# Kernel tuning notes

Measured on AMD Instinct MI355X. Metric: run time of the kernel, lower is better.

## Reference

```python
import jax, jax.numpy as jnp
import numpy as np

B_, L_, O_, N_, S_, U_, DEL, HID, K = 16, 128, 128, 256, 64, 32, 64, 512, 4
D_OUT = DEL + N_ * U_ + N_ * S_  # 24640


def setup_inputs() -> dict:
    key = jax.random.key(0)
    ks = jax.random.split(key, 12)
    return {
        "x": jax.random.normal(ks[0], (B_, O_ + L_, S_), jnp.float32),
        "u": jax.random.normal(ks[1], (B_, 2 * L_, U_), jnp.float32),
        "A": jax.random.normal(ks[2], (N_, 1), jnp.float32) / 20.0,
        "W0": jax.random.normal(ks[3], (HID, S_), jnp.float32) * 0.05,
        "b0": jnp.zeros((HID,), jnp.float32),
        "W1": jax.random.normal(ks[4], (N_, HID), jnp.float32) * 0.05,
        "b1": jnp.zeros((N_,), jnp.float32),
        "conv_w": jax.random.normal(ks[5], (N_ + U_, 1, K), jnp.float32) * 0.3,
        "conv_b": jnp.zeros((N_ + U_,), jnp.float32),
        "Wg": jax.random.normal(ks[6], (D_OUT, N_ + U_), jnp.float32) * 0.05,
        "bg": jnp.zeros((D_OUT,), jnp.float32),
        "Wdt": jax.random.normal(ks[7], (N_, DEL), jnp.float32) * 0.05,
        "bdt": jnp.zeros((N_,), jnp.float32),
    }


def reference(x, u, A, W0, b0, W1, b1, conv_w, conv_b, Wg, bg, Wdt, bdt):
    def proj_x(v):  # Linear -> relu -> Linear (project_x)
        return jax.nn.relu(v @ W0.T + b0) @ W1.T + b1

    u = u[:, :, :U_]
    z0 = proj_x(x[:, O_ - 1, :])                       # (B, N)

    # ---- generate_matrices ----
    x_all = proj_x(x[:, :O_ - 1, :])                   # (B, O-1, N)
    u_all = u[:, :O_ - 1, :]                           # (B, O-1, U)
    old = jax.nn.silu(jnp.concatenate([x_all, u_all], axis=2))  # (B, O-1, N+U)
    old = jnp.transpose(old, (0, 2, 1))                # (B, N+U, O-1)
    old = jax.lax.conv_general_dilated(
        old, conv_w, window_strides=(1,), padding=[(K - 1, K - 1)],
        dimension_numbers=("NCH", "OIH", "NCH"), feature_group_count=N_ + U_,
    ) + conv_b[None, :, None]
    old = old[:, :, -L_:]                              # last L timesteps
    old = jax.nn.silu(jnp.transpose(old, (0, 2, 1)))   # (B, L, N+U)
    gen = old @ Wg.T + bg                              # (B, L, delta + N*U + N*S)
    delta, Bm, Cm = jnp.split(gen, [DEL, DEL + N_ * U_], axis=-1)
    delta = jax.nn.softplus(delta @ Wdt.T + bdt)       # (B, L, N)
    Bm = Bm.reshape(B_, L_, N_, U_)
    Cm = Cm.reshape(B_, L_, N_, S_)

    # ---- discretion_matrices ----
    a = A[:, 0]
    a = -jnp.where(a > 0, a, jnp.expm1(a))             # -celu(A), alpha=1
    dA = jnp.exp(delta * a)                            # (B, L, N)
    dB = ((dA - 1.0) * (1.0 / a))[..., None] * Bm      # (B, L, N, U)

    # ---- selective_scan ----
    u0 = u[:, O_ - 1:O_ - 1 + L_, :]                   # (B, L, U)
    xt = x[:, O_:O_ + L_, :]                           # (B, L, S) targets

    def step(z, inp):
        dAi, dBi, ui, Ci, xti = inp
        z = z * dAi + jnp.einsum("bnu,bu->bn", dBi, ui)
        y = jnp.einsum("bns,bn->bs", Ci, z)
        return z, (y, jnp.mean((y - xti) ** 2))

    xs = (
        jnp.swapaxes(dA, 0, 1), jnp.swapaxes(dB, 0, 1),
        jnp.swapaxes(u0, 0, 1), jnp.swapaxes(Cm, 0, 1), jnp.swapaxes(xt, 0, 1),
    )
    _, (ys, ls) = jax.lax.scan(step, z0, xs)
    loss = jnp.sum(ls) / L_
    return loss, jax.lax.stop_gradient(ys)             # ys: (L, B, S), detached as in torch
```

## Files before the change

### kernel.cpp

```cpp
#include <hip/hip_runtime.h>
#include <math.h>

#define B_   16
#define L_   128
#define O_   128
#define N_   256
#define S_   64
#define U_   32
#define DEL_ 64
#define HID_ 512
#define CH_  288
#define M_   2048
#define KD_  288
#define CM_BASE (DEL_ + N_*U_)
#define NSLICE 32

typedef __bf16 bf16_t;
typedef bf16_t bf16x8 __attribute__((ext_vector_type(8)));
typedef float  f32x4  __attribute__((ext_vector_type(4)));

#define AS1(p) ((const __attribute__((address_space(1))) void*)(unsigned long long)(const void*)(p))
#define AS3(p) ((__attribute__((address_space(3))) void*)(unsigned int)(unsigned long long)(const void*)(p))

__device__ __forceinline__ float silu_f(float x){ return x / (1.f + expf(-x)); }
__device__ __forceinline__ float softplus_f(float x){
  return fmaxf(x, 0.f) + log1pf(expf(-fabsf(x)));
}

__device__ __forceinline__ void cvt8(const float* src, bf16_t* dst){
  float4 a = ((const float4*)src)[0];
  float4 b = ((const float4*)src)[1];
  bf16x8 o;
  o[0]=(bf16_t)a.x; o[1]=(bf16_t)a.y; o[2]=(bf16_t)a.z; o[3]=(bf16_t)a.w;
  o[4]=(bf16_t)b.x; o[5]=(bf16_t)b.y; o[6]=(bf16_t)b.z; o[7]=(bf16_t)b.w;
  *(bf16x8*)dst = o;
}

#define CVT_BLOCKS 3465
#define W0_BLOCKS  16
#define W1_BLOCKS  64
#define XB_BLOCKS  64
#define WGT_BLOCKS 72
__global__ void k_prep(const float* __restrict__ Wg, bf16_t* __restrict__ Wgbf,
                       const float* __restrict__ W0, bf16_t* __restrict__ W0bf,
                       const float* __restrict__ W1, bf16_t* __restrict__ W1bf,
                       const float* __restrict__ x,  bf16_t* __restrict__ xbf,
                       float* __restrict__ WgdT, float* __restrict__ lossa){
  if (blockIdx.x == 0 && threadIdx.x < 2) lossa[threadIdx.x] = 0.f;
  if (blockIdx.x < CVT_BLOCKS) {
    int i = blockIdx.x*256 + threadIdx.x;
    if (i >= 887040) return;
    cvt8(Wg + (size_t)i*8, Wgbf + (size_t)i*8);
  } else if (blockIdx.x < CVT_BLOCKS + W0_BLOCKS) {
    int i = (blockIdx.x - CVT_BLOCKS)*256 + threadIdx.x;
    if (i >= 4096) return;
    cvt8(W0 + (size_t)i*8, W0bf + (size_t)i*8);
  } else if (blockIdx.x < CVT_BLOCKS + W0_BLOCKS + W1_BLOCKS) {
    int i = (blockIdx.x - CVT_BLOCKS - W0_BLOCKS)*256 + threadIdx.x;
    if (i >= 16384) return;
    cvt8(W1 + (size_t)i*8, W1bf + (size_t)i*8);
  } else if (blockIdx.x < CVT_BLOCKS + W0_BLOCKS + W1_BLOCKS + XB_BLOCKS) {
    int i = (blockIdx.x - CVT_BLOCKS - W0_BLOCKS - W1_BLOCKS)*256 + threadIdx.x;
    if (i >= 16384) return;
    int m = i >> 3, c0 = (i & 7)*8;
    int b = m >> 7, t = m & 127;
    cvt8(x + (size_t)(((b<<8)+t)<<6) + c0, xbf + (size_t)m*64 + c0);
  } else {
    int i = (blockIdx.x - CVT_BLOCKS - W0_BLOCKS - W1_BLOCKS - XB_BLOCKS)*256 + threadIdx.x;
    if (i >= 18432) return;
    int d = i / KD_, k = i - d*KD_;
    WgdT[k*64 + d] = Wg[(size_t)d*KD_ + k];
  }
}

#define STAGE64K(GBASE, ROW0G, STRIDE, KK, LDSP)                                     \
  { const bf16_t* gp_ = (GBASE) + (size_t)((ROW0G) + wave*16 + lm)*(STRIDE) + (KK) + lq*8; \
    __builtin_amdgcn_global_load_lds(AS1(gp_), AS3((LDSP) + wave*512), 16, 0, 0); }

#define STAGE128(GBASE, ROW0G, STRIDE, TT, BUF)                                      \
  { _Pragma("unroll")                                                                \
    for (int kb_ = 0; kb_ < 4; kb_++) {                                              \
      const bf16_t* gp_ = (GBASE) + (size_t)((ROW0G) + wave*16 + lm)*(STRIDE)        \
                          + (TT)*128 + kb_*32 + lq*8;                                \
      __builtin_amdgcn_global_load_lds(AS1(gp_), AS3((BUF) + kb_*2048 + wave*512), 16, 0, 0);\
    } }

#define STAGE32(GBASE, ROW0G, KK, LDSP)                                              \
  { _Pragma("unroll")                                                                \
    for (int l_ = 0; l_ < 2; l_++) {                                                 \
      int g_ = wave*2 + l_;                                                          \
      const bf16_t* gp_ = (GBASE) + (size_t)((ROW0G) + g_*16 + lm)*KD_ + (KK) + lq*8;\
      __builtin_amdgcn_global_load_lds(AS1(gp_), AS3((LDSP) + g_*512), 16, 0, 0);    \
    } }

#define STAGE_FR96(GBASE, ROW0G, KK, LDSP)                                           \
  { _Pragma("unroll")                                                                \
    for (int c_ = 0; c_ < 3; c_++) {                                                 \
      _Pragma("unroll")                                                              \
      for (int q_ = 0; q_ < 2; q_++) {                                               \
        int g_ = wave*2 + q_;                                                        \
        const bf16_t* gp_ = (GBASE) + (size_t)((ROW0G) + g_*16 + lm)*KD_ + (KK) + c_*32 + lq*8;\
        __builtin_amdgcn_global_load_lds(AS1(gp_), AS3((LDSP) + c_*4096 + g_*512), 16, 0, 0);\
      } } }

__global__ __launch_bounds__(256) void k_mlp1m(
    const bf16_t* __restrict__ xbf, const bf16_t* __restrict__ W0bf,
    const float* __restrict__ b0, bf16_t* __restrict__ Hbf){
  __shared__ __align__(16) bf16_t As[2][2048];
  __shared__ __align__(16) bf16_t Bs[2][2048];
  int tid = threadIdx.x;
  int wave = tid >> 6, lane = tid & 63;
  int wm = wave & 1, wn = wave >> 1;
  int nt = blockIdx.x, mt = blockIdx.y;
  int m0 = mt*64, n0 = nt*64;
  int lm = lane & 15, lq = lane >> 4;

  f32x4 acc[2][2];
  #pragma unroll
  for (int i=0;i<2;i++)
    #pragma unroll
    for (int j=0;j<2;j++){ acc[i][j][0]=0.f;acc[i][j][1]=0.f;acc[i][j][2]=0.f;acc[i][j][3]=0.f; }

  STAGE64K(xbf,  m0, 64, 0, As[0]);
  STAGE64K(W0bf, n0, 64, 0, Bs[0]);
  __syncthreads();
  #pragma unroll
  for (int t = 0; t < 2; ++t) {
    int cur = t & 1;
    if (t < 1) {
      STAGE64K(xbf,  m0, 64, 32, As[1]);
      STAGE64K(W0bf, n0, 64, 32, Bs[1]);
    }
    bf16x8 af[2], bff[2];
    #pragma unroll
    for (int i=0;i<2;i++) af[i]  = *(const bf16x8*)&As[cur][(wm*2 + i)*512 + lane*8];
    #pragma unroll
    for (int j=0;j<2;j++) bff[j] = *(const bf16x8*)&Bs[cur][(wn*2 + j)*512 + lane*8];
    #pragma unroll
    for (int i=0;i<2;i++)
      #pragma unroll
      for (int j=0;j<2;j++)
        acc[i][j] = __builtin_amdgcn_mfma_f32_16x16x32_bf16(af[i], bff[j], acc[i][j], 0,0,0);
    __syncthreads();
  }
  #pragma unroll
  for (int i=0;i<2;i++)
    #pragma unroll
    for (int j=0;j<2;j++){
      int col = n0 + wn*32 + j*16 + lm;
      float bb = b0[col];
      #pragma unroll
      for (int r=0;r<4;r++){
        int row = m0 + wm*32 + i*16 + lq*4 + r;
        Hbf[(size_t)row*HID_ + col] = (bf16_t)fmaxf(acc[i][j][r] + bb, 0.f);
      }
    }
}

__global__ __launch_bounds__(256) void k_mlp2m(
    const bf16_t* __restrict__ Hbf, const bf16_t* __restrict__ W1bf,
    const float* __restrict__ b1, float* __restrict__ P){
  __shared__ __align__(16) bf16_t As[2][8192];
  __shared__ __align__(16) bf16_t Bs[2][8192];
  int tid = threadIdx.x;
  int wave = tid >> 6, lane = tid & 63;
  int wm = wave & 1, wn = wave >> 1;
  int nt = blockIdx.x, mt = blockIdx.y;
  int m0 = mt*64, n0 = nt*64;
  int lm = lane & 15, lq = lane >> 4;

  f32x4 acc[2][2];
  #pragma unroll
  for (int i=0;i<2;i++)
    #pragma unroll
    for (int j=0;j<2;j++){ acc[i][j][0]=0.f;acc[i][j][1]=0.f;acc[i][j][2]=0.f;acc[i][j][3]=0.f; }

  STAGE128(Hbf,  m0, HID_, 0, As[0]);
  STAGE128(W1bf, n0, HID_, 0, Bs[0]);
  __syncthreads();
  #pragma unroll
  for (int t = 0; t < 4; ++t) {
    int cur = t & 1;
    if (t < 3) {
      STAGE128(Hbf,  m0, HID_, t+1, As[cur^1]);
      STAGE128(W1bf, n0, HID_, t+1, Bs[cur^1]);
    }
    #pragma unroll
    for (int kb = 0; kb < 4; kb++) {
      bf16x8 af[2], bff[2];
      #pragma unroll
      for (int i=0;i<2;i++) af[i]  = *(const bf16x8*)&As[cur][kb*2048 + (wm*2 + i)*512 + lane*8];
      #pragma unroll
      for (int j=0;j<2;j++) bff[j] = *(const bf16x8*)&Bs[cur][kb*2048 + (wn*2 + j)*512 + lane*8];
      #pragma unroll
      for (int i=0;i<2;i++)
        #pragma unroll
        for (int j=0;j<2;j++)
          acc[i][j] = __builtin_amdgcn_mfma_f32_16x16x32_bf16(af[i], bff[j], acc[i][j], 0,0,0);
    }
    __syncthreads();
  }
  #pragma unroll
  for (int i=0;i<2;i++)
    #pragma unroll
    for (int j=0;j<2;j++){
      int col = n0 + wn*32 + j*16 + lm;
      float bb = b1[col];
      #pragma unroll
      for (int r=0;r<4;r++){
        int row = m0 + wm*32 + i*16 + lq*4 + r;
        P[(size_t)row*N_ + col] = acc[i][j][r] + bb;
      }
    }
}

__global__ __launch_bounds__(256) void k_convdelta(
    const float* __restrict__ P, const float* __restrict__ u,
    const float* __restrict__ cw, const float* __restrict__ cb,
    const float* __restrict__ WgdT, const float* __restrict__ bg,
    const float* __restrict__ Wdt, const float* __restrict__ bdt,
    const float* __restrict__ Ap, bf16_t* __restrict__ oldbf,
    float* __restrict__ dA, float* __restrict__ coef){
  __shared__ __align__(16) float olds[4*KD_];
  __shared__ float dr[4][64];
  int tid = threadIdx.x;
  int m0 = blockIdx.x * 4;
  int b = m0 >> 7, l0 = m0 & 127;
  for (int e = tid; e < 4*CH_; e += 256) {
    int r = e / CH_, c = e - r*CH_;
    int l = l0 + r;
    float acc = cb[c];
    #pragma unroll
    for (int k = 0; k < 4; k++) {
      int t = l + k - 1;
      if (t >= 0 && t <= O_-2) {
        float s = (c < N_) ? P[((b<<7)+t)*N_ + c] : u[((b<<8)+t)*U_ + (c-N_)];
        acc += silu_f(s) * cw[c*4 + k];
      }
    }
    float v = silu_f(acc);
    olds[e] = v;
    oldbf[(size_t)(m0+r)*CH_ + c] = (bf16_t)v;
  }
  __syncthreads();
  {
    int d = tid & 63;
    int r = tid >> 6;
    const float* wcol = WgdT + d;
    const float* orow = olds + r*KD_;
    float s = 0.f;
    for (int k = 0; k < KD_; k++) s += orow[k] * wcol[k*64];
    dr[r][d] = s + bg[d];
  }
  __syncthreads();
  int n = tid;
  float wrow[64];
  {
    const float4* wd4 = (const float4*)(Wdt + (size_t)n*64);
    #pragma unroll
    for (int q = 0; q < 16; q++) {
      float4 w = wd4[q];
      wrow[q*4+0]=w.x; wrow[q*4+1]=w.y; wrow[q*4+2]=w.z; wrow[q*4+3]=w.w;
    }
  }
  float a0 = Ap[n];
  float a = -(a0 > 0.f ? a0 : expm1f(a0));
  float inva = 1.f / a;
  float bd = bdt[n];
  #pragma unroll
  for (int r = 0; r < 4; r++) {
    float s = bd;
    #pragma unroll
    for (int d = 0; d < 64; d++) s += dr[r][d] * wrow[d];
    float dd = softplus_f(s);
    float e  = expf(dd * a);
    size_t m = m0 + r;
    dA[m*N_ + n]   = e;
    coef[m*N_ + n] = (e - 1.f) * inva;
  }
}

__global__ __launch_bounds__(256, 2) void k_bmfma(
    const bf16_t* __restrict__ oldbf, const bf16_t* __restrict__ Wgbf,
    const float* __restrict__ bg, const float* __restrict__ u,
    const float* __restrict__ coef, const float* __restrict__ dAg,
    const float* __restrict__ Pg, float* __restrict__ zall){
  __shared__ union {
    struct { __align__(16) bf16_t A[2][4096]; __align__(16) bf16_t B[2][4096]; } st;
    struct { float wl[128][4]; float dal[128][4]; } sc;
  } sm;
  int tid = threadIdx.x;
  int wave = tid >> 6, lane = tid & 63;
  int wm = wave & 1, wn = wave >> 1;
  int mt = blockIdx.y, nt = blockIdx.x;
  int m0 = mt*128, ncol0 = nt*128;
  int lm = lane & 15, lq = lane >> 4;

  f32x4 acc[4][4];
  #pragma unroll
  for (int i=0;i<4;i++)
    #pragma unroll
    for (int j=0;j<4;j++){ acc[i][j][0]=0.f;acc[i][j][1]=0.f;acc[i][j][2]=0.f;acc[i][j][3]=0.f; }

  STAGE32(oldbf, m0, 0, sm.st.A[0]);
  STAGE32(Wgbf, DEL_ + ncol0, 0, sm.st.B[0]);
  __syncthreads();
  for (int t = 0; t < 9; ++t) {
    int cur = t & 1;
    if (t < 8) {
      int kk = (t+1)*32;
      STAGE32(oldbf, m0, kk, sm.st.A[cur^1]);
      STAGE32(Wgbf, DEL_ + ncol0, kk, sm.st.B[cur^1]);
    }
    bf16x8 af[4], bff[4];
    #pragma unroll
    for (int i=0;i<4;i++) af[i]  = *(const bf16x8*)&sm.st.A[cur][(wm*4 + i)*512 + lane*8];
    #pragma unroll
    for (int j=0;j<4;j++) bff[j] = *(const bf16x8*)&sm.st.B[cur][(wn*4 + j)*512 + lane*8];
    __builtin_amdgcn_s_setprio(1);
    #pragma unroll
    for (int i=0;i<4;i++)
      #pragma unroll
      for (int j=0;j<4;j++)
        acc[i][j] = __builtin_amdgcn_mfma_f32_16x16x32_bf16(af[i], bff[j], acc[i][j], 0,0,0);
    __builtin_amdgcn_s_setprio(0);
    __syncthreads();
  }

  for (int e = tid; e < 512; e += 256)
    sm.sc.dal[e>>2][e&3] = dAg[(size_t)(m0 + (e>>2))*N_ + nt*4 + (e&3)];

  float bgv[4];
  #pragma unroll
  for (int j=0;j<4;j++) bgv[j] = bg[DEL_ + ncol0 + wn*64 + j*16 + lm];
  float p[2][4][4];
  #pragma unroll
  for (int a=0;a<2;a++)
    #pragma unroll
    for (int i=0;i<4;i++)
      #pragma unroll
      for (int r=0;r<4;r++) p[a][i][r]=0.f;
  #pragma unroll
  for (int i=0;i<4;i++){
    #pragma unroll
    for (int r=0;r<4;r++){
      int m = m0 + wm*64 + i*16 + lq*4 + r;
      int b = m >> 7, l = m & 127;
      const float* urow = u + ((size_t)(b<<8) + 127 + l)*U_;
      #pragma unroll
      for (int j=0;j<4;j++){
        float uu = urow[(j&1)*16 + lm];
        p[j>>1][i][r] += (acc[i][j][r] + bgv[j]) * uu;
      }
    }
  }
  #pragma unroll
  for (int mk = 1; mk < 16; mk <<= 1){
    #pragma unroll
    for (int a=0;a<2;a++)
      #pragma unroll
      for (int i=0;i<4;i++)
        #pragma unroll
        for (int r=0;r<4;r++) p[a][i][r] += __shfl_xor(p[a][i][r], mk);
  }
  if (lm == 0){
    #pragma unroll
    for (int nl=0;nl<2;nl++){
      int n = ((ncol0 + wn*64 + nl*32) >> 5);
      int nc = wn*2 + nl;
      #pragma unroll
      for (int i=0;i<4;i++)
        #pragma unroll
        for (int r=0;r<4;r++){
          int l = wm*64 + i*16 + lq*4 + r;
          sm.sc.wl[l][nc] = coef[(size_t)(m0+l)*N_ + n] * p[nl][i][r];
        }
    }
  }
  __syncthreads();

  {
    int nc = wave;
    int n = nt*4 + nc;
    float z0 = Pg[(size_t)(m0 + 127)*N_ + n];
    int l0 = lane*2;
    float a0 = sm.sc.dal[l0][nc],   w0 = sm.sc.wl[l0][nc];
    float a1 = sm.sc.dal[l0+1][nc], w1 = sm.sc.wl[l0+1][nc];
    float A = a0*a1, Bv = w0*a1 + w1;
    #pragma unroll
    for (int d = 1; d < 64; d <<= 1){
      float Ap = __shfl_up(A, d);
      float Bp = __shfl_up(Bv, d);
      if (lane >= d){ Bv = Bp*A + Bv; A = Ap*A; }
    }
    float Ae = __shfl_up(A, 1);
    float Be = __shfl_up(Bv, 1);
    if (lane == 0){ Ae = 1.f; Be = 0.f; }
    float zp = z0*Ae + Be;
    float za = zp*a0 + w0;
    float zb = za*a1 + w1;
    zall[(size_t)(m0 + l0)*N_ + n]     = za;
    zall[(size_t)(m0 + l0 + 1)*N_ + n] = zb;
  }
}

__global__ __launch_bounds__(256, 2) void k_cmfma(
    const bf16_t* __restrict__ oldbf, const bf16_t* __restrict__ Wgbf,
    const float* __restrict__ bg, const float* __restrict__ zall,
    float* __restrict__ ypart){
  __shared__ union {
    struct { __align__(16) bf16_t A[3*4096];
             __align__(16) bf16_t Bb[4][4096];
             float zl[128][8]; } st;
    float ylds[128][64];
  } sm;
  int tid = threadIdx.x;
  int wave = tid >> 6, lane = tid & 63;
  int wm = wave & 1, wn = wave >> 1;
  int mt = blockIdx.y, grp = blockIdx.x;
  int m0 = mt*128;
  int lm = lane & 15, lq = lane >> 4;

  for (int e = tid; e < 1024; e += 256)
    sm.st.zl[e>>3][e&7] = zall[(size_t)(m0 + (e>>3))*N_ + grp*8 + (e&7)];

  f32x4 yacc[4][4];
  #pragma unroll
  for (int i=0;i<4;i++)
    #pragma unroll
    for (int j=0;j<4;j++){ yacc[i][j][0]=0.f;yacc[i][j][1]=0.f;yacc[i][j][2]=0.f;yacc[i][j][3]=0.f; }

  f32x4 acc[4][4];
  for (int kh = 0; kh < 3; kh++) {
    int kk = kh*96;
    if (kh) __builtin_amdgcn_s_barrier();
    STAGE_FR96(oldbf, m0, kk, sm.st.A);
    STAGE32(Wgbf, CM_BASE + (grp*4)*128, kk,      sm.st.Bb[0]);
    STAGE32(Wgbf, CM_BASE + (grp*4)*128, kk + 32, sm.st.Bb[1]);
    asm volatile("s_waitcnt vmcnt(0)" ::: "memory");
    __builtin_amdgcn_s_barrier();

    #pragma unroll
    for (int c = 0; c < 12; ++c) {
      int it = c/3, cb = c%3;
      if (c + 2 < 12) {
        int c2 = c + 2, it2 = c2/3, cb2 = c2%3;
        STAGE32(Wgbf, CM_BASE + (grp*4 + it2)*128, kk + cb2*32, sm.st.Bb[c2 & 3]);
      }
      if (c <= 9)       { asm volatile("s_waitcnt vmcnt(4)" ::: "memory"); }
      else if (c == 10) { asm volatile("s_waitcnt vmcnt(2)" ::: "memory"); }
      else              { asm volatile("s_waitcnt vmcnt(0)" ::: "memory"); }
      __builtin_amdgcn_s_barrier();
      if (cb == 0) {
        #pragma unroll
        for (int i=0;i<4;i++)
          #pragma unroll
          for (int j=0;j<4;j++){ acc[i][j][0]=0.f;acc[i][j][1]=0.f;acc[i][j][2]=0.f;acc[i][j][3]=0.f; }
      }
      bf16x8 af[4], bff[4];
      #pragma unroll
      for (int i=0;i<4;i++) af[i]  = *(const bf16x8*)&sm.st.A[cb*4096 + (wm*4 + i)*512 + lane*8];
      #pragma unroll
      for (int j=0;j<4;j++) bff[j] = *(const bf16x8*)&sm.st.Bb[c & 3][(wn*4 + j)*512 + lane*8];
      __builtin_amdgcn_s_setprio(1);
      #pragma unroll
      for (int i=0;i<4;i++)
        #pragma unroll
        for (int j=0;j<4;j++)
          acc[i][j] = __builtin_amdgcn_mfma_f32_16x16x32_bf16(af[i], bff[j], acc[i][j], 0,0,0);
      __builtin_amdgcn_s_setprio(0);
      if (cb == 2) {
        int ncol0 = (grp*4 + it)*128;
        int nl = it*2 + wn;
        float bgv[4];
        #pragma unroll
        for (int j=0;j<4;j++)
          bgv[j] = (kh == 2) ? bg[CM_BASE + ncol0 + wn*64 + j*16 + lm] : 0.f;
        #pragma unroll
        for (int i=0;i<4;i++){
          #pragma unroll
          for (int r=0;r<4;r++){
            float zv = sm.st.zl[wm*64 + i*16 + lq*4 + r][nl];
            #pragma unroll
            for (int j=0;j<4;j++)
              yacc[i][j][r] += (acc[i][j][r] + bgv[j]) * zv;
          }
        }
      }
    }
  }

  __builtin_amdgcn_s_barrier();
  if (wn == 1){
    #pragma unroll
    for (int i=0;i<4;i++)
      #pragma unroll
      for (int j=0;j<4;j++)
        #pragma unroll
        for (int r=0;r<4;r++){
          int ml = wm*64 + i*16 + lq*4 + r;
          sm.ylds[ml][j*16 + lm] = yacc[i][j][r];
        }
  }
  __syncthreads();
  if (wn == 0){
    float* dst = ypart + (size_t)grp*(M_*S_);
    #pragma unroll
    for (int i=0;i<4;i++)
      #pragma unroll
      for (int j=0;j<4;j++)
        #pragma unroll
        for (int r=0;r<4;r++){
          int ml = wm*64 + i*16 + lq*4 + r;
          int s = j*16 + lm;
          dst[(size_t)(m0+ml)*S_ + s] = yacc[i][j][r] + sm.ylds[ml][s];
        }
  }
}

__global__ void k_finalize(const float* __restrict__ ypart, const float* __restrict__ x,
                           float* __restrict__ out, float* __restrict__ lossacc){
  __shared__ float red[256];
  int tid = threadIdx.x;
  float ls = 0.f;
  #pragma unroll
  for (int q = 0; q < 2; q++) {
    int e = blockIdx.x*512 + q*256 + tid;
    int m = e >> 6, s = e & 63;
    int b = m >> 7, l = m & 127;
    float yv = 0.f;
    #pragma unroll 8
    for (int g = 0; g < NSLICE; g++) yv += ypart[(size_t)g*(M_*S_) + e];
    out[1 + (size_t)((l<<4) + b)*S_ + s] = yv;
    float xv = x[((size_t)(b<<8) + 128 + l)*S_ + s];
    float d = yv - xv;
    ls += d*d;
  }
  red[tid] = ls; __syncthreads();
  for (int st = 128; st > 0; st >>= 1) {
    if (tid < st) red[tid] += red[tid+st];
    __syncthreads();
  }
  if (tid == 0) {
    atomicAdd(&lossacc[0], red[0]);
    __threadfence();
    unsigned old = atomicAdd((unsigned*)&lossacc[1], 1u);
    if (old == 255u) {
      float tot = atomicAdd(&lossacc[0], 0.f);
      out[0] = tot * (1.f / (float)(B_*S_*L_));
    }
  }
}

extern "C" void kernel_launch(void* const* d_in, const int* in_sizes, int n_in,
                              void* d_out, int out_size, void* d_ws, size_t ws_size,
                              hipStream_t stream) {
  const float* x   = (const float*)d_in[0];
  const float* u   = (const float*)d_in[1];
  const float* Ap  = (const float*)d_in[2];
  const float* W0  = (const float*)d_in[3];
  const float* b0  = (const float*)d_in[4];
  const float* W1  = (const float*)d_in[5];
  const float* b1  = (const float*)d_in[6];
  const float* cw  = (const float*)d_in[7];
  const float* cb  = (const float*)d_in[8];
  const float* Wg  = (const float*)d_in[9];
  const float* bg  = (const float*)d_in[10];
  const float* Wdt = (const float*)d_in[11];
  const float* bdt = (const float*)d_in[12];
  float* out = (float*)d_out;

  float* ws    = (float*)d_ws;
  float* zall  = ws;
  float* lossa = zall + 524288;
  bf16_t* oldbf = (bf16_t*)(lossa + 512);
  bf16_t* Wgbf  = (bf16_t*)(lossa + 512 + 294912);
  bf16_t* W0bf  = (bf16_t*)(lossa + 512 + 294912 + 3548160);
  bf16_t* W1bf  = (bf16_t*)(lossa + 512 + 294912 + 3548160 + 16384);
  bf16_t* xbf   = (bf16_t*)(lossa + 512 + 294912 + 3548160 + 16384 + 65536);
  bf16_t* Hbf   = (bf16_t*)(lossa + 512 + 294912 + 3548160 + 16384 + 65536 + 65536);
  float* R     = lossa + 512 + 294912 + 3548160 + 16384 + 65536 + 65536 + 524288;
  float* Pp    = R;
  float* dA    = Pp   + 524288;
  float* coef  = dA   + 524288;
  float* ypart = R;
  float* WgdT  = R + 4194304;

  k_prep<<<CVT_BLOCKS + W0_BLOCKS + W1_BLOCKS + XB_BLOCKS + WGT_BLOCKS, 256, 0, stream>>>(
      Wg, Wgbf, W0, W0bf, W1, W1bf, x, xbf, WgdT, lossa);
  k_mlp1m<<<dim3(HID_/64, M_/64), 256, 0, stream>>>(xbf, W0bf, b0, Hbf);
  k_mlp2m<<<dim3(N_/64, M_/64), 256, 0, stream>>>(Hbf, W1bf, b1, Pp);
  k_convdelta<<<M_/4, 256, 0, stream>>>(Pp, u, cw, cb, WgdT, bg, Wdt, bdt, Ap,
                                        oldbf, dA, coef);
  k_bmfma<<<dim3(64, 16), 256, 0, stream>>>(oldbf, Wgbf, bg, u, coef, dA, Pp, zall);
  k_cmfma<<<dim3(32, 16), 256, 0, stream>>>(oldbf, Wgbf, bg, zall, ypart);
  k_finalize<<<256, 256, 0, stream>>>(ypart, x, out, lossa);
}
```

Baseline: 192.1 us.

## Deepen k_bmfma LDS pipeline to 4 buffers and transpose Wdt for coalescing

```diff
diff --git a/kernel.cpp b/kernel.cpp
--- a/kernel.cpp
+++ b/kernel.cpp
@@ -41,10 +41,12 @@
 #define W1_BLOCKS  64
 #define XB_BLOCKS  64
 #define WGT_BLOCKS 72
+#define WDT_BLOCKS 64
 __global__ void k_prep(const float* __restrict__ Wg, bf16_t* __restrict__ Wgbf,
                        const float* __restrict__ W0, bf16_t* __restrict__ W0bf,
                        const float* __restrict__ W1, bf16_t* __restrict__ W1bf,
                        const float* __restrict__ x,  bf16_t* __restrict__ xbf,
+                       const float* __restrict__ Wdt, float* __restrict__ WdtT,
                        float* __restrict__ WgdT, float* __restrict__ lossa){
   if (blockIdx.x == 0 && threadIdx.x < 2) lossa[threadIdx.x] = 0.f;
   if (blockIdx.x < CVT_BLOCKS) {
@@ -65,11 +67,16 @@
     int m = i >> 3, c0 = (i & 7)*8;
     int b = m >> 7, t = m & 127;
     cvt8(x + (size_t)(((b<<8)+t)<<6) + c0, xbf + (size_t)m*64 + c0);
-  } else {
+  } else if (blockIdx.x < CVT_BLOCKS + W0_BLOCKS + W1_BLOCKS + XB_BLOCKS + WGT_BLOCKS) {
     int i = (blockIdx.x - CVT_BLOCKS - W0_BLOCKS - W1_BLOCKS - XB_BLOCKS)*256 + threadIdx.x;
     if (i >= 18432) return;
     int d = i / KD_, k = i - d*KD_;
     WgdT[k*64 + d] = Wg[(size_t)d*KD_ + k];
+  } else {
+    int i = (blockIdx.x - CVT_BLOCKS - W0_BLOCKS - W1_BLOCKS - XB_BLOCKS - WGT_BLOCKS)*256 + threadIdx.x;
+    if (i >= 16384) return;
+    int d = i >> 8, n = i & 255;
+    WdtT[i] = Wdt[(size_t)n*64 + d];
   }
 }
 
@@ -218,7 +225,7 @@
     const float* __restrict__ P, const float* __restrict__ u,
     const float* __restrict__ cw, const float* __restrict__ cb,
     const float* __restrict__ WgdT, const float* __restrict__ bg,
-    const float* __restrict__ Wdt, const float* __restrict__ bdt,
+    const float* __restrict__ WdtT, const float* __restrict__ bdt,
     const float* __restrict__ Ap, bf16_t* __restrict__ oldbf,
     float* __restrict__ dA, float* __restrict__ coef){
   __shared__ __align__(16) float olds[4*KD_];
@@ -255,14 +262,8 @@
   __syncthreads();
   int n = tid;
   float wrow[64];
-  {
-    const float4* wd4 = (const float4*)(Wdt + (size_t)n*64);
-    #pragma unroll
-    for (int q = 0; q < 16; q++) {
-      float4 w = wd4[q];
-      wrow[q*4+0]=w.x; wrow[q*4+1]=w.y; wrow[q*4+2]=w.z; wrow[q*4+3]=w.w;
-    }
-  }
+  #pragma unroll
+  for (int d = 0; d < 64; d++) wrow[d] = WdtT[d*256 + n];
   float a0 = Ap[n];
   float a = -(a0 > 0.f ? a0 : expm1f(a0));
   float inva = 1.f / a;
@@ -286,7 +287,7 @@
     const float* __restrict__ coef, const float* __restrict__ dAg,
     const float* __restrict__ Pg, float* __restrict__ zall){
   __shared__ union {
-    struct { __align__(16) bf16_t A[2][4096]; __align__(16) bf16_t B[2][4096]; } st;
+    struct { __align__(16) bf16_t A[4][4096]; __align__(16) bf16_t B[4][4096]; } st;
     struct { float wl[128][4]; float dal[128][4]; } sc;
   } sm;
   int tid = threadIdx.x;
@@ -304,19 +305,24 @@
 
   STAGE32(oldbf, m0, 0, sm.st.A[0]);
   STAGE32(Wgbf, DEL_ + ncol0, 0, sm.st.B[0]);
-  __syncthreads();
+  STAGE32(oldbf, m0, 32, sm.st.A[1]);
+  STAGE32(Wgbf, DEL_ + ncol0, 32, sm.st.B[1]);
+  #pragma unroll
   for (int t = 0; t < 9; ++t) {
-    int cur = t & 1;
-    if (t < 8) {
-      int kk = (t+1)*32;
-      STAGE32(oldbf, m0, kk, sm.st.A[cur^1]);
-      STAGE32(Wgbf, DEL_ + ncol0, kk, sm.st.B[cur^1]);
-    }
+    if (t + 2 < 9) {
+      int kk = (t+2)*32;
+      STAGE32(oldbf, m0, kk, sm.st.A[(t+2)&3]);
+      STAGE32(Wgbf, DEL_ + ncol0, kk, sm.st.B[(t+2)&3]);
+    }
+    if (t <= 6)      { asm volatile("s_waitcnt vmcnt(8)" ::: "memory"); }
+    else if (t == 7) { asm volatile("s_waitcnt vmcnt(4)" ::: "memory"); }
+    else             { asm volatile("s_waitcnt vmcnt(0)" ::: "memory"); }
+    __builtin_amdgcn_s_barrier();
     bf16x8 af[4], bff[4];
     #pragma unroll
-    for (int i=0;i<4;i++) af[i]  = *(const bf16x8*)&sm.st.A[cur][(wm*4 + i)*512 + lane*8];
-    #pragma unroll
-    for (int j=0;j<4;j++) bff[j] = *(const bf16x8*)&sm.st.B[cur][(wn*4 + j)*512 + lane*8];
+    for (int i=0;i<4;i++) af[i]  = *(const bf16x8*)&sm.st.A[t&3][(wm*4 + i)*512 + lane*8];
+    #pragma unroll
+    for (int j=0;j<4;j++) bff[j] = *(const bf16x8*)&sm.st.B[t&3][(wn*4 + j)*512 + lane*8];
     __builtin_amdgcn_s_setprio(1);
     #pragma unroll
     for (int i=0;i<4;i++)
@@ -324,8 +330,8 @@
       for (int j=0;j<4;j++)
         acc[i][j] = __builtin_amdgcn_mfma_f32_16x16x32_bf16(af[i], bff[j], acc[i][j], 0,0,0);
     __builtin_amdgcn_s_setprio(0);
-    __syncthreads();
-  }
+  }
+  __syncthreads();
 
   for (int e = tid; e < 512; e += 256)
     sm.sc.dal[e>>2][e&3] = dAg[(size_t)(m0 + (e>>2))*N_ + nt*4 + (e&3)];
@@ -585,12 +591,14 @@
   float* coef  = dA   + 524288;
   float* ypart = R;
   float* WgdT  = R + 4194304;
-
-  k_prep<<<CVT_BLOCKS + W0_BLOCKS + W1_BLOCKS + XB_BLOCKS + WGT_BLOCKS, 256, 0, stream>>>(
-      Wg, Wgbf, W0, W0bf, W1, W1bf, x, xbf, WgdT, lossa);
+  float* WdtT  = WgdT + 18432;
+
+  k_prep<<<CVT_BLOCKS + W0_BLOCKS + W1_BLOCKS + XB_BLOCKS + WGT_BLOCKS + WDT_BLOCKS,
+           256, 0, stream>>>(
+      Wg, Wgbf, W0, W0bf, W1, W1bf, x, xbf, Wdt, WdtT, WgdT, lossa);
   k_mlp1m<<<dim3(HID_/64, M_/64), 256, 0, stream>>>(xbf, W0bf, b0, Hbf);
   k_mlp2m<<<dim3(N_/64, M_/64), 256, 0, stream>>>(Hbf, W1bf, b1, Pp);
-  k_convdelta<<<M_/4, 256, 0, stream>>>(Pp, u, cw, cb, WgdT, bg, Wdt, bdt, Ap,
+  k_convdelta<<<M_/4, 256, 0, stream>>>(Pp, u, cw, cb, WgdT, bg, WdtT, bdt, Ap,
                                         oldbf, dA, coef);
   k_bmfma<<<dim3(64, 16), 256, 0, stream>>>(oldbf, Wgbf, bg, u, coef, dA, Pp, zall);
   k_cmfma<<<dim3(32, 16), 256, 0, stream>>>(oldbf, Wgbf, bg, zall, ypart);
```

Measured after the change: 191.9 us. Within noise of the previous version (-0.1%).
